# Kernel tuning notes

Measured on AMD Instinct MI355X. Metric: run time of the kernel, lower is better.

The kernel has to match this reference:

```python
import jax, jax.numpy as jnp
import numpy as np

CONF_THRES = 0.1
IOU_THRES = 0.6
MAX_DET = 300
MAX_WH = 4096.0  # class offset for non-agnostic NMS
NEG_SLOPE = 0.01  # nn.LeakyReLU default


def xywh2xyxy(p):
    xy, wh = p[..., :2], p[..., 2:4]
    return jnp.concatenate([xy - wh / 2, xy + wh / 2], axis=-1)


def pairwise_iou(a, b):
    area_a = (a[:, 2] - a[:, 0]) * (a[:, 3] - a[:, 1])
    area_b = (b[:, 2] - b[:, 0]) * (b[:, 3] - b[:, 1])
    lt = jnp.maximum(a[:, None, :2], b[None, :, :2])
    rb = jnp.minimum(a[:, None, 2:], b[None, :, 2:])
    wh = jnp.clip(rb - lt, 0.0)
    inter = wh[..., 0] * wh[..., 1]
    return inter / (area_a[:, None] + area_b[None, :] - inter + 1e-7)


def nms_single(pred):  # pred: [N, 5+nc]
    boxes = xywh2xyxy(pred[:, :4])
    scores = pred[:, 5:] * pred[:, 4:5]  # obj * cls
    conf = jnp.max(scores, axis=1)
    cls = jnp.argmax(scores, axis=1)
    conf = jnp.where(conf > CONF_THRES, conf, 0.0)
    topv, topi = jax.lax.top_k(conf, MAX_DET)
    b = boxes[topi]                      # [K,4]
    c = cls[topi]
    valid = topv > CONF_THRES
    bo = b + (c.astype(b.dtype) * MAX_WH)[:, None]  # class-offset boxes
    iou = pairwise_iou(bo, bo)           # [K,K]
    idx = jnp.arange(MAX_DET)
    def body(i, keep):
        sup = keep[i] & (iou[i] > IOU_THRES) & (idx > i)
        return keep & ~sup
    keep = jax.lax.fori_loop(0, MAX_DET, body, valid)
    return b, keep


def bilinear_sample(feat, y, x):  # feat [C,H,W], y/x [K,P] -> [C,K,P]
    C, H, W = feat.shape
    y = jnp.clip(y, 0.0, H - 1.0)
    x = jnp.clip(x, 0.0, W - 1.0)
    y0 = jnp.floor(y).astype(jnp.int32)
    x0 = jnp.floor(x).astype(jnp.int32)
    y1 = jnp.minimum(y0 + 1, H - 1)
    x1 = jnp.minimum(x0 + 1, W - 1)
    ly = y - y0
    lx = x - x0
    return (feat[:, y0, x0] * ((1 - ly) * (1 - lx))
            + feat[:, y0, x1] * ((1 - ly) * lx)
            + feat[:, y1, x0] * (ly * (1 - lx))
            + feat[:, y1, x1] * (ly * lx))


def roi_align_1x1(feat, boxes, scale):  # feat [C,H,W], boxes [K,4] xyxy (input-px)
    b = boxes * scale
    w = jnp.maximum(b[:, 2] - b[:, 0], 1.0)
    h = jnp.maximum(b[:, 3] - b[:, 1], 1.0)
    off = jnp.array([0.5, 1.5], dtype=boxes.dtype)
    xs = b[:, 0:1] + off[None, :] * (w[:, None] / 2.0)  # [K,2]
    ys = b[:, 1:2] + off[None, :] * (h[:, None] / 2.0)
    yy = ys[:, jnp.array([0, 0, 1, 1])]  # [K,4] 2x2 grid
    xx = xs[:, jnp.array([0, 1, 0, 1])]
    v = bilinear_sample(feat, yy, xx)    # [C,K,4]
    return jnp.mean(v, axis=2).T         # [K,C]


def rescale_boxes(bbox, hw, hw0):  # scale_coords + normalize by orig shape
    gain = jnp.minimum(hw[0] / hw0[0], hw[1] / hw0[1])
    pad_x = (hw[1] - hw0[1] * gain) / 2.0
    pad_y = (hw[0] - hw0[0] * gain) / 2.0
    x1 = jnp.clip((bbox[:, 0] - pad_x) / gain, 0.0, hw0[1])
    y1 = jnp.clip((bbox[:, 1] - pad_y) / gain, 0.0, hw0[0])
    x2 = jnp.clip((bbox[:, 2] - pad_x) / gain, 0.0, hw0[1])
    y2 = jnp.clip((bbox[:, 3] - pad_y) / gain, 0.0, hw0[0])
    # divide by shapes[i][0] indexed [w,h,w,h]
    return jnp.stack([x1 / hw0[1], y1 / hw0[0], x2 / hw0[1], y2 / hw0[0]], axis=1)


def setup_inputs() -> dict:
    key = jax.random.key(0)
    ks = jax.random.split(key, 10)
    B, N, NC = 8, 25500, 80
    xy = jax.random.uniform(ks[0], (B, N, 2), minval=0.0, maxval=640.0)
    wh = jax.random.uniform(ks[1], (B, N, 2), minval=8.0, maxval=160.0)
    obj = jax.random.uniform(ks[2], (B, N, 1))
    cls = jax.random.uniform(ks[3], (B, N, NC))
    preds = jnp.concatenate([xy, wh, obj, cls], axis=-1)
    feat1 = jax.random.normal(ks[4], (B, 128, 80, 80), dtype=jnp.float32)
    feat2 = jax.random.normal(ks[5], (B, 256, 40, 40), dtype=jnp.float32)
    feat3 = jax.random.normal(ks[6], (B, 512, 20, 20), dtype=jnp.float32)
    feat4 = jax.random.normal(ks[7], (B, 1024, 10, 10), dtype=jnp.float32)
    orig_hw = jnp.tile(jnp.array([[720.0, 1280.0]], dtype=jnp.float32), (B, 1))
    W1 = jax.random.normal(ks[8], (1920, 256), dtype=jnp.float32) * 0.02
    b1 = jnp.zeros((256,), dtype=jnp.float32)
    W2 = jax.random.normal(ks[9], (256, 256), dtype=jnp.float32) * 0.02
    b2 = jnp.zeros((256,), dtype=jnp.float32)
    return {"preds": preds, "feat1": feat1, "feat2": feat2, "feat3": feat3,
            "feat4": feat4, "orig_hw": orig_hw, "W1": W1, "b1": b1,
            "W2": W2, "b2": b2}


def reference(preds, feat1, feat2, feat3, feat4, orig_hw, W1, b1, W2, b2):
    preds = jax.lax.stop_gradient(preds)  # out.detach() in the original
    hw = jnp.array(feat1.shape[-2:], dtype=preds.dtype) * 8.0  # network input h,w
    boxes, keep = jax.vmap(nms_single)(preds)  # [B,K,4], [B,K]
    f1 = jax.vmap(lambda f, b: roi_align_1x1(f, b, 1.0 / 8))(feat1, boxes)
    f2 = jax.vmap(lambda f, b: roi_align_1x1(f, b, 1.0 / 16))(feat2, boxes)
    f3 = jax.vmap(lambda f, b: roi_align_1x1(f, b, 1.0 / 32))(feat3, boxes)
    f4 = jax.vmap(lambda f, b: roi_align_1x1(f, b, 1.0 / 64))(feat4, boxes)
    f = jnp.concatenate([f1, f2, f3, f4], axis=-1)  # [B,K,1920]
    h = jax.nn.leaky_relu(f @ W1 + b1, NEG_SLOPE)
    h = jax.nn.leaky_relu(h @ W2 + b2, NEG_SLOPE)   # [B,K,256]
    bb = jax.vmap(lambda b, s: rescale_boxes(b, hw, s))(boxes, orig_hw)
    out = jnp.concatenate([bb, h], axis=-1)  # [B,K,260]
    return out * keep[..., None].astype(out.dtype)
```

## Files before the change

### kernel.cpp

```cpp
#include <hip/hip_runtime.h>
#include <hip/hip_bf16.h>
#include <cstdint>
#include <cstddef>

#define NBATCH 8
#define NANCH 25500
#define MAXDET 300
#define NBINS 2048
#define CAP 2048

typedef __bf16 bf16x8 __attribute__((ext_vector_type(8)));
typedef float floatx4 __attribute__((ext_vector_type(4)));
typedef unsigned long long ull;

__device__ __forceinline__ int conf_bin(float v) {
  unsigned bits = __float_as_uint(v);
  int bin = (int)((bits - 0x3D800000u) >> 14);
  return bin > (NBINS - 1) ? (NBINS - 1) : bin;
}

#define CONF_TILE 64
__global__ __launch_bounds__(256) void conf_kernel(const float* __restrict__ preds,
                                                   float* __restrict__ conf,
                                                   int* __restrict__ cls, int total) {
  __shared__ float s[CONF_TILE * 85];
  int base = blockIdx.x * CONF_TILE;
  int nA = total - base; if (nA > CONF_TILE) nA = CONF_TILE;
  int n4 = (nA * 85) >> 2;
  const float4* g4 = (const float4*)(preds + (size_t)base * 85);
  float4* s4 = (float4*)s;
  for (int i = threadIdx.x; i < n4; i += 256) s4[i] = g4[i];
  __syncthreads();
  int lane16 = threadIdx.x & 15;
  int sub = threadIdx.x >> 4;
  #pragma unroll
  for (int r = 0; r < 4; ++r) {
    int a = r * 16 + sub;
    if (a < nA) {
      const float* row = s + a * 85;
      float obj = row[4];
      float best = -1.0f; int bc = 0;
      #pragma unroll
      for (int j = 0; j < 5; ++j) {
        int c = lane16 * 5 + j;
        float v = row[5 + c] * obj;
        if (v > best) { best = v; bc = c; }
      }
      #pragma unroll
      for (int m = 1; m < 16; m <<= 1) {
        float ov = __shfl_xor(best, m, 64);
        int   oc = __shfl_xor(bc,   m, 64);
        if (ov > best || (ov == best && oc < bc)) { best = ov; bc = oc; }
      }
      if (lane16 == 0) {
        int idx = base + a;
        conf[idx] = (best > 0.1f) ? best : 0.0f;
        cls[idx] = bc;
      }
    }
  }
}

struct TransArgs {
  const float* src[6];
  __hip_bfloat16* dst[6];
  int C[6], HW[6], tx[6], tpb[6], start[6];
};

__global__ __launch_bounds__(1024) void mid_kernel(TransArgs a,
                                                   const float* __restrict__ conf,
                                                   const float* __restrict__ preds,
                                                   const int* __restrict__ clsg,
                                                   float* __restrict__ cand_v, int* __restrict__ cand_i,
                                                   float* __restrict__ boxesWs, int* __restrict__ keepWs,
                                                   const float* __restrict__ orig_hw,
                                                   float* __restrict__ out,
                                                   int n_trans_tiles) {
  #pragma clang fp contract(off)
  __shared__ __align__(16) char smem[69632];
  int bid = blockIdx.x;
  int t = threadIdx.y * 32 + threadIdx.x;

  if (bid >= 8) {
    int wv = t >> 6, l = t & 63;
    int wid = (bid - 8) * 16 + wv;
    int wtot = ((int)gridDim.x - 8) * 16;
    float* tile = (float*)(smem + wv * 4352);
    for (int gt = wid; gt < n_trans_tiles; gt += wtot) {
      int s = 0;
      #pragma unroll
      for (int i = 1; i < 6; ++i) if (gt >= a.start[i]) s = i;
      int local = gt - a.start[s];
      int C = a.C[s], HW = a.HW[s], tx0 = a.tx[s], tpb = a.tpb[s];
      int bb = local / tpb;
      int rem = local - bb * tpb;
      int p0 = (rem % tx0) * 32;
      int c0 = (rem / tx0) * 32;
      const float* inb = a.src[s] + (size_t)bb * C * HW;
      __hip_bfloat16* outb = a.dst[s] + (size_t)bb * C * HW;
      if (p0 + 32 <= HW) {
        #pragma unroll
        for (int k = 0; k < 4; ++k) {
          int cr = k * 8 + (l >> 3);
          int pr = (l & 7) * 4;
          float4 v = *(const float4*)(inb + (size_t)(c0 + cr) * HW + p0 + pr);
          float* d = tile + cr * 33 + pr;
          d[0] = v.x; d[1] = v.y; d[2] = v.z; d[3] = v.w;
        }
        asm volatile("s_waitcnt lgkmcnt(0)" ::: "memory");
        __builtin_amdgcn_sched_barrier(0);
        #pragma unroll
        for (int k = 0; k < 16; ++k) {
          int pr = k * 2 + (l >> 5);
          int cr = l & 31;
          outb[(size_t)(p0 + pr) * C + c0 + cr] = __float2bfloat16(tile[cr * 33 + pr]);
        }
      } else {
        int nvp = HW - p0;
        #pragma unroll
        for (int k = 0; k < 4; ++k) {
          int cr = k * 8 + (l >> 3);
          int pr = (l & 7) * 4;
          const float* src = inb + (size_t)(c0 + cr) * HW + p0;
          float* d = tile + cr * 33 + pr;
          #pragma unroll
          for (int j = 0; j < 4; ++j) d[j] = (pr + j < nvp) ? src[pr + j] : 0.0f;
        }
        asm volatile("s_waitcnt lgkmcnt(0)" ::: "memory");
        __builtin_amdgcn_sched_barrier(0);
        #pragma unroll
        for (int k = 0; k < 16; ++k) {
          int pr = k * 2 + (l >> 5);
          int cr = l & 31;
          if (pr < nvp) outb[(size_t)(p0 + pr) * C + c0 + cr] = __float2bfloat16(tile[cr * 33 + pr]);
        }
      }
    }
    return;
  }

  int b = bid;
  int*    s_h  = (int*)smem;
  int*    s_ctr= (int*)(smem + 8192);
  ull   (*mask)[5] = (ull(*)[5])smem;
  float*  lv_s = (float*)(smem + 16384);
  int*    li_s = (int*)(smem + 24576);
  float4* bo4  = (float4*)(smem + 32768);
  float (*bxx)[4] = (float(*)[4])(smem + 37568);
  ull* keepw = (ull*)(smem + 42368);
  ull* nzrow = (ull*)(smem + 42408);
  int* shv   = (int*)(smem + 42448);

  s_h[t] = 0; s_h[t + 1024] = 0;
  if (t < 300) {
    bo4[t] = make_float4(0.0f, 0.0f, 0.0f, 0.0f);
    bxx[t][0] = 0.0f; bxx[t][1] = 0.0f; bxx[t][2] = 0.0f; bxx[t][3] = 0.0f;
  }
  if (t < 5) nzrow[t] = 0ULL;
  if (t == 1) { shv[0] = NBINS; shv[2] = 0; }
  __syncthreads();

  {
    const float4* cf4 = (const float4*)(conf + (size_t)b * NANCH);
    const int N4 = NANCH >> 2;
    for (int i = t; i < N4; i += 1024) {
      float4 v = cf4[i];
      if (v.x > 0.1f) atomicAdd(&s_h[conf_bin(v.x)], 1);
      if (v.y > 0.1f) atomicAdd(&s_h[conf_bin(v.y)], 1);
      if (v.z > 0.1f) atomicAdd(&s_h[conf_bin(v.z)], 1);
      if (v.w > 0.1f) atomicAdd(&s_h[conf_bin(v.w)], 1);
    }
  }
  __syncthreads();

  int r[8], suf[8], rs[8];
  int w = t >> 6, lane = t & 63;
  if (t < 256) {
    #pragma unroll
    for (int k = 0; k < 8; ++k)
      r[k] = s_h[(w * 8 + k) * 64 + lane];
    int bsum = 0;
    #pragma unroll
    for (int k = 0; k < 8; ++k) {
      int s = r[k];
      #pragma unroll
      for (int d = 1; d < 64; d <<= 1) {
        int o = __shfl_down(s, d, 64);
        if (lane + d < 64) s += o;
      }
      suf[k] = s - r[k];
      rs[k] = __shfl(s, 0, 64);
      bsum += rs[k];
    }
    if (lane == 0) shv[4 + w] = bsum;
  }
  __syncthreads();
  if (t < 256) {
    int p1 = shv[5], p2 = shv[6], p3 = shv[7];
    int total = shv[4] + p1 + p2 + p3;
    int target = total < 300 ? total : 300;
    int RS = (w == 0) ? (p1 + p2 + p3) : (w == 1) ? (p2 + p3) : (w == 2) ? p3 : 0;
    int run = RS;
    #pragma unroll
    for (int k = 7; k >= 0; --k) {
      int Sx = run + suf[k] + r[k];
      int Sx1 = Sx - r[k];
      int bin = (w * 8 + k) * 64 + lane;
      s_h[bin] = Sx;
      s_ctr[bin] = Sx1;
      if (total > 0 && Sx >= target && Sx1 < target) { shv[0] = bin; shv[2] = Sx; }
      run += rs[k];
    }
    if (t == 0) shv[1] = total;
  }
  __syncthreads();
  int T = shv[0];
  int total = shv[1];
  int Kslots = shv[2];
  int nvalid = total < 300 ? total : 300;

  if (t >= nvalid && t < 300) {
    size_t bi = ((size_t)(b * 300 + t)) * 4;
    boxesWs[bi + 0] = 0.0f; boxesWs[bi + 1] = 0.0f;
    boxesWs[bi + 2] = 0.0f; boxesWs[bi + 3] = 0.0f;
  }
  if (t < 5) {
    int n = nvalid - t * 64;
    keepw[t] = (n <= 0) ? 0ULL : (n >= 64 ? ~0ULL : ((1ULL << n) - 1ULL));
  }

  {
    const float4* cf4 = (const float4*)(conf + (size_t)b * NANCH);
    const int N4 = NANCH >> 2;
    float* cv = cand_v + (size_t)b * NANCH;
    int*   ci = cand_i + (size_t)b * NANCH;
    if (total > 0) {
      for (int i4 = t; i4 < N4; i4 += 1024) {
        float4 v4 = cf4[i4];
        int i0 = i4 * 4;
        float vv[4] = {v4.x, v4.y, v4.z, v4.w};
        #pragma unroll
        for (int q = 0; q < 4; ++q) {
          float v = vv[q];
          if (v > 0.1f) {
            int bin = conf_bin(v);
            if (bin >= T) {
              int slot = atomicAdd(&s_ctr[bin], 1);
              if (slot < CAP) { lv_s[slot] = v; li_s[slot] = i0 + q; }
              else            { cv[slot] = v;   ci[slot] = i0 + q;   }
            }
          }
        }
      }
    }
  }
  __syncthreads();

  {
    const float* cv = cand_v + (size_t)b * NANCH;
    const int*   ci = cand_i + (size_t)b * NANCH;
    for (int sIdx = t; sIdx < Kslots; sIdx += 1024) {
      float v; int id;
      if (sIdx < CAP) { v = lv_s[sIdx]; id = li_s[sIdx]; }
      else            { v = cv[sIdx];   id = ci[sIdx];   }
      int bin = conf_bin(v);
      int lo = (bin + 1 < NBINS) ? s_h[bin + 1] : 0;
      int hi = s_h[bin];
      int rank = lo;
      for (int j = lo; j < hi; ++j) {
        float vj; int ij;
        if (j < CAP) { vj = lv_s[j]; ij = li_s[j]; }
        else         { vj = cv[j];   ij = ci[j];   }
        rank += (int)((vj > v) | ((vj == v) & (ij < id)));
      }
      if (rank < 300) {
        const float* p = preds + ((size_t)b * NANCH + id) * 85;
        float cx = p[0], cy = p[1], wq = p[2], hq = p[3];
        float hw2 = wq * 0.5f, hh2 = hq * 0.5f;
        float x1 = cx - hw2, y1 = cy - hh2, x2 = cx + hw2, y2 = cy + hh2;
        bxx[rank][0] = x1; bxx[rank][1] = y1; bxx[rank][2] = x2; bxx[rank][3] = y2;
        size_t bi = ((size_t)(b * 300 + rank)) * 4;
        boxesWs[bi + 0] = x1; boxesWs[bi + 1] = y1;
        boxesWs[bi + 2] = x2; boxesWs[bi + 3] = y2;
        int c = clsg[(size_t)b * NANCH + id];
        float off = (float)c * 4096.0f;
        float4 ob; ob.x = x1 + off; ob.y = y1 + off; ob.z = x2 + off; ob.w = y2 + off;
        bo4[rank] = ob;
      }
    }
  }
  __syncthreads();

  {
    int wv2 = t >> 6, ln = t & 63;
    if (wv2 < 10) {
      int w2 = wv2 >> 1, half = wv2 & 1;
      int j = w2 * 64 + ln;
      int jc = j < 300 ? j : 0;
      float4 jb = bo4[jc];
      float ja = (jb.z - jb.x) * (jb.w - jb.y);
      bool jv = j < 300;
      int iend = w2 * 64 + 64; if (iend > 300) iend = 300;
      int i0 = half * 150, i1 = i0 + 150; if (i1 > iend) i1 = iend;
      #pragma unroll 4
      for (int i = i0; i < i1; ++i) {
        float4 ib = bo4[i];
        float ai = (ib.z - ib.x) * (ib.w - ib.y);
        float ltx = fmaxf(ib.x, jb.x);
        float lty = fmaxf(ib.y, jb.y);
        float rbx = fminf(ib.z, jb.z);
        float rby = fminf(ib.w, jb.w);
        float wx = fmaxf(rbx - ltx, 0.0f);
        float wy = fmaxf(rby - lty, 0.0f);
        float inter = wx * wy;
        float iou = inter / (ai + ja - inter + 1e-7f);
        ull bal = __ballot(jv && (j > i) && (iou > 0.6f));
        if (ln == 0) {
          mask[i][w2] = bal;
          if (bal) atomicOr(&nzrow[i >> 6], 1ULL << (i & 63));
        }
      }
    }
  }
  __syncthreads();
  if (t == 0) {
    ull kw[5], nz[5];
    #pragma unroll
    for (int w2 = 0; w2 < 5; ++w2) { kw[w2] = keepw[w2]; nz[w2] = nzrow[w2]; }
    #pragma unroll
    for (int w2 = 0; w2 < 5; ++w2) {
      ull p = kw[w2] & nz[w2];
      while (p) {
        int l2 = __builtin_ctzll(p);
        p &= p - 1;
        int i = w2 * 64 + l2;
        for (int w3 = w2; w3 < 5; ++w3) {
          ull m = mask[i][w3];
          kw[w3] &= ~m;
          if (w3 == w2) p &= ~m;
        }
      }
    }
    #pragma unroll
    for (int w2 = 0; w2 < 5; ++w2) keepw[w2] = kw[w2];
  }
  __syncthreads();
  if (t < 300) {
    int kp = (int)((keepw[t >> 6] >> (t & 63)) & 1ULL);
    keepWs[b * 300 + t] = kp;
    float oh = orig_hw[b * 2 + 0], ow = orig_hw[b * 2 + 1];
    float gain = fminf(640.0f / oh, 640.0f / ow);
    float padx = (640.0f - ow * gain) * 0.5f;
    float pady = (640.0f - oh * gain) * 0.5f;
    float x1 = fminf(fmaxf((bxx[t][0] - padx) / gain, 0.0f), ow) / ow;
    float y1 = fminf(fmaxf((bxx[t][1] - pady) / gain, 0.0f), oh) / oh;
    float x2 = fminf(fmaxf((bxx[t][2] - padx) / gain, 0.0f), ow) / ow;
    float y2 = fminf(fmaxf((bxx[t][3] - pady) / gain, 0.0f), oh) / oh;
    size_t o = ((size_t)(b * 300 + t)) * 260;
    out[o + 0] = kp ? x1 : 0.0f;
    out[o + 1] = kp ? y1 : 0.0f;
    out[o + 2] = kp ? x2 : 0.0f;
    out[o + 3] = kp ? y2 : 0.0f;
  }
}

__global__ __launch_bounds__(256) void roi_kernel(const float* __restrict__ boxes,
                                                  const __hip_bfloat16* __restrict__ fT1, const __hip_bfloat16* __restrict__ fT2,
                                                  const __hip_bfloat16* __restrict__ fT3, const __hip_bfloat16* __restrict__ fT4,
                                                  __hip_bfloat16* __restrict__ f) {
  int b = blockIdx.x & 7;
  int r = blockIdx.x >> 3;
  __shared__ int t_off[4][16];
  __shared__ float t_w[4][16];
  int t = threadIdx.x;
  const int Hs[4] = {80, 40, 20, 10};
  const int Cs[4] = {128, 256, 512, 1024};
  const float ss[4] = {0.125f, 0.0625f, 0.03125f, 0.015625f};
  size_t bbase = ((size_t)(b * 300 + r)) * 4;
  float bx0 = boxes[bbase + 0];
  float by0 = boxes[bbase + 1];
  float bx1 = boxes[bbase + 2];
  float by1 = boxes[bbase + 3];
  if (t < 64) {
    int lv = t >> 4, k = t & 15, pp = k >> 2, nb = k & 3;
    float s = ss[lv];
    int H = Hs[lv], W = Hs[lv], C = Cs[lv];
    float b0 = bx0 * s, b1 = by0 * s, b2 = bx1 * s, b3 = by1 * s;
    float w = fmaxf(b2 - b0, 1.0f), h = fmaxf(b3 - b1, 1.0f);
    const float offv[2] = {0.5f, 1.5f};
    float px = b0 + offv[pp & 1] * (w * 0.5f);
    float py = b1 + offv[pp >> 1] * (h * 0.5f);
    float y = fminf(fmaxf(py, 0.0f), (float)(H - 1));
    float x = fminf(fmaxf(px, 0.0f), (float)(W - 1));
    int y0 = (int)floorf(y), x0 = (int)floorf(x);
    int y1 = min(y0 + 1, H - 1), x1 = min(x0 + 1, W - 1);
    float ly = y - (float)y0, lx = x - (float)x0;
    int yy = (nb & 2) ? y1 : y0;
    int xx = (nb & 1) ? x1 : x0;
    float wy = (nb & 2) ? ly : (1.0f - ly);
    float wx = (nb & 1) ? lx : (1.0f - lx);
    t_off[lv][k] = (yy * W + xx) * C;
    t_w[lv][k] = wy * wx;
  }
  __syncthreads();
  const __hip_bfloat16* bases[4] = {
    fT1 + (size_t)b * 6400 * 128,
    fT2 + (size_t)b * 1600 * 256,
    fT3 + (size_t)b * 400 * 512,
    fT4 + (size_t)b * 100 * 1024
  };
  __hip_bfloat16* frow = f + (size_t)(b * 300 + r) * 1920;
  int cbase = 0;
  #pragma unroll
  for (int lv = 0; lv < 4; ++lv) {
    int C = Cs[lv];
    const __hip_bfloat16* base = bases[lv];
    for (int c = t; c < C; c += 256) {
      float acc = 0.0f;
      #pragma unroll
      for (int k = 0; k < 16; ++k)
        acc += t_w[lv][k] * __bfloat162float(base[t_off[lv][k] + c]);
      frow[cbase + c] = __float2bfloat16(acc * 0.25f);
    }
    cbase += C;
  }
}

#define GLDS16(gp, lp) __builtin_amdgcn_global_load_lds( \
    (const __attribute__((address_space(1))) unsigned int*)(gp), \
    (__attribute__((address_space(3))) unsigned int*)(lp), 16, 0, 0)

__global__ __launch_bounds__(256) void gemm_tile_kernel(const __hip_bfloat16* __restrict__ A,
                                                        const __hip_bfloat16* __restrict__ BT,
                                                        const float* __restrict__ bias,
                                                        __hip_bfloat16* __restrict__ Cb,
                                                        float* __restrict__ Cf,
                                                        const int* __restrict__ keep,
                                                        int M, int N, int K, int ldc, int coff) {
  __shared__ __hip_bfloat16 sA[2][64 * 64];
  __shared__ __hip_bfloat16 sB[2][64 * 64];
  int tid = threadIdx.x;
  int bm = blockIdx.x * 64, bn = blockIdx.y * 64;
  int wave = tid >> 6, lane = tid & 63;
  int wr = wave >> 1, wc = wave & 1;
  int idx16 = lane & 15, kb = lane >> 4;
  floatx4 acc[2][2] = {};
  int nt = K >> 6;

  auto stage = [&](int buf, int t) {
    int k0 = t << 6;
    #pragma unroll
    for (int i = 0; i < 2; ++i) {
      int c = tid + i * 256;
      int row = c >> 3, cc = c & 7;
      int scc = cc ^ (row & 7);
      GLDS16(A + (size_t)(bm + row) * K + k0 + scc * 8,
             (char*)&sA[buf][0] + c * 16);
    }
    #pragma unroll
    for (int i = 0; i < 2; ++i) {
      int c = tid + i * 256;
      int row = c >> 3, cc = c & 7;
      int scc = cc ^ (row & 7);
      GLDS16(BT + (size_t)(bn + row) * K + k0 + scc * 8,
             (char*)&sB[buf][0] + c * 16);
    }
  };

  stage(0, 0);
  asm volatile("s_waitcnt vmcnt(0)" ::: "memory");
  __syncthreads();
  int cur = 0;
  for (int t = 0; t < nt; ++t) {
    if (t + 1 < nt) stage(cur ^ 1, t + 1);
    const char* Ab = (const char*)&sA[cur][0];
    const char* Bb = (const char*)&sB[cur][0];
    #pragma unroll
    for (int s = 0; s < 2; ++s) {
      bf16x8 af[2], bg[2];
      #pragma unroll
      for (int m = 0; m < 2; ++m) {
        int row = wr * 32 + m * 16 + idx16;
        int chunk = s * 4 + kb;
        af[m] = *(const bf16x8*)(Ab + row * 128 + ((chunk ^ (row & 7)) * 16));
      }
      #pragma unroll
      for (int n = 0; n < 2; ++n) {
        int row = wc * 32 + n * 16 + idx16;
        int chunk = s * 4 + kb;
        bg[n] = *(const bf16x8*)(Bb + row * 128 + ((chunk ^ (row & 7)) * 16));
      }
      #pragma unroll
      for (int m = 0; m < 2; ++m)
        #pragma unroll
        for (int n = 0; n < 2; ++n)
          acc[m][n] = __builtin_amdgcn_mfma_f32_16x16x32_bf16(af[m], bg[n], acc[m][n], 0, 0, 0);
    }
    asm volatile("s_waitcnt vmcnt(0)" ::: "memory");
    __syncthreads();
    cur ^= 1;
  }
  int col = lane & 15, rb4 = (lane >> 4) * 4;
  #pragma unroll
  for (int m = 0; m < 2; ++m) {
    #pragma unroll
    for (int n = 0; n < 2; ++n) {
      #pragma unroll
      for (int r = 0; r < 4; ++r) {
        int orow = bm + wr * 32 + m * 16 + rb4 + r;
        int ocol = bn + wc * 32 + n * 16 + col;
        if (orow >= M) continue;
        float v = acc[m][n][r] + bias[ocol];
        v = (v >= 0.0f) ? v : 0.01f * v;
        if (Cb) Cb[(size_t)orow * N + ocol] = __float2bfloat16(v);
        if (Cf) {
          float km = keep ? (keep[orow] ? 1.0f : 0.0f) : 1.0f;
          Cf[(size_t)orow * ldc + coff + ocol] = v * km;
        }
      }
    }
  }
}

extern "C" void kernel_launch(void* const* d_in, const int* in_sizes, int n_in,
                              void* d_out, int out_size, void* d_ws, size_t ws_size,
                              hipStream_t stream) {
  (void)in_sizes; (void)n_in; (void)out_size; (void)ws_size;
  const float* preds  = (const float*)d_in[0];
  const float* feat1  = (const float*)d_in[1];
  const float* feat2  = (const float*)d_in[2];
  const float* feat3  = (const float*)d_in[3];
  const float* feat4  = (const float*)d_in[4];
  const float* orighw = (const float*)d_in[5];
  const float* W1     = (const float*)d_in[6];
  const float* b1     = (const float*)d_in[7];
  const float* W2     = (const float*)d_in[8];
  const float* b2     = (const float*)d_in[9];
  float* out = (float*)d_out;

  char* ws = (char*)d_ws;
  size_t off = 0;
  auto alloc = [&](size_t bytes) -> void* {
    void* p = ws + off;
    off = (off + bytes + 255) & ~(size_t)255;
    return p;
  };
  const int BN = NBATCH * NANCH;
  float*  conf   = (float*)alloc((size_t)BN * 4);
  int*    cls    = (int*)  alloc((size_t)BN * 4);
  float*  cand_v = (float*)alloc((size_t)BN * 4);
  int*    cand_i = (int*)  alloc((size_t)BN * 4);
  float*  boxes  = (float*)alloc((size_t)NBATCH * 300 * 4 * 4);
  int*    keep   = (int*)  alloc((size_t)NBATCH * 300 * 4);
  __hip_bfloat16* fT1  = (__hip_bfloat16*)alloc((size_t)NBATCH * 6400 * 128 * 2);
  __hip_bfloat16* fT2  = (__hip_bfloat16*)alloc((size_t)NBATCH * 1600 * 256 * 2);
  __hip_bfloat16* fT3  = (__hip_bfloat16*)alloc((size_t)NBATCH * 400 * 512 * 2);
  __hip_bfloat16* fT4  = (__hip_bfloat16*)alloc((size_t)NBATCH * 100 * 1024 * 2);
  __hip_bfloat16* fmat = (__hip_bfloat16*)alloc((size_t)2400 * 1920 * 2);
  __hip_bfloat16* h1b  = (__hip_bfloat16*)alloc((size_t)2400 * 256 * 2);
  __hip_bfloat16* W1T  = (__hip_bfloat16*)alloc((size_t)256 * 1920 * 2);
  __hip_bfloat16* W2T  = (__hip_bfloat16*)alloc((size_t)256 * 256 * 2);

  conf_kernel<<<(BN + CONF_TILE - 1) / CONF_TILE, 256, 0, stream>>>(preds, conf, cls, BN);

  TransArgs ta;
  ta.src[0] = feat1; ta.dst[0] = fT1; ta.C[0] = 128;  ta.HW[0] = 6400; ta.tx[0] = 200;
  ta.src[1] = feat2; ta.dst[1] = fT2; ta.C[1] = 256;  ta.HW[1] = 1600; ta.tx[1] = 50;
  ta.src[2] = feat3; ta.dst[2] = fT3; ta.C[2] = 512;  ta.HW[2] = 400;  ta.tx[2] = 13;
  ta.src[3] = feat4; ta.dst[3] = fT4; ta.C[3] = 1024; ta.HW[3] = 100;  ta.tx[3] = 4;
  ta.src[4] = W1;    ta.dst[4] = W1T; ta.C[4] = 1920; ta.HW[4] = 256;  ta.tx[4] = 8;
  ta.src[5] = W2;    ta.dst[5] = W2T; ta.C[5] = 256;  ta.HW[5] = 256;  ta.tx[5] = 8;
  int n_tiles = 0;
  for (int s = 0; s < 6; ++s) {
    int ty = (ta.C[s] + 31) / 32;
    int nbatch = (s < 4) ? NBATCH : 1;
    ta.tpb[s] = ta.tx[s] * ty;
    ta.start[s] = n_tiles;
    n_tiles += ta.tpb[s] * nbatch;
  }
  mid_kernel<<<8 + 432, dim3(32, 32), 0, stream>>>(ta, conf, preds, cls,
                                                   cand_v, cand_i, boxes, keep, orighw, out,
                                                   n_tiles);

  roi_kernel<<<2400, 256, 0, stream>>>(boxes, fT1, fT2, fT3, fT4, fmat);
  gemm_tile_kernel<<<dim3(38, 4), 256, 0, stream>>>(fmat, W1T, b1, h1b, nullptr, nullptr,
                                                    2400, 256, 1920, 0, 0);
  gemm_tile_kernel<<<dim3(38, 4), 256, 0, stream>>>(h1b, W2T, b2, nullptr, out, keep,
                                                    2400, 256, 256, 260, 4);
}
```

Before: 121.0 us.

## Move histogram into conf kernel and parallelize candidate scatter across helper blocks

The per-batch confidence histogram is now built with global atomics inside the conf kernel instead of by one block per batch in the mid kernel. 64 new helper blocks (8 per batch) each compute the threshold bin and scatter the candidates from one segment into bin-sorted global slots, packing score, index, class and box into 64-bit words. The NMS blocks spin on a per-batch counter until the helpers finish, then rank the candidates from global memory. This removes the serial 25.5k-element scan done by a single block per batch. In exchange it adds a memset, global atomics, an inter-block spin-wait that assumes the helper blocks are co-resident, and atomic reads of global memory during ranking.

```diff
diff --git a/kernel.cpp b/kernel.cpp
--- a/kernel.cpp
+++ b/kernel.cpp
@@ -7,7 +7,10 @@
 #define NANCH 25500
 #define MAXDET 300
 #define NBINS 2048
-#define CAP 2048
+#define NMS_BLKS 8
+#define SCAT_BLKS 64
+#define TRANS_BASE (NMS_BLKS + SCAT_BLKS)
+#define TRANS_BLKS 376
 
 typedef __bf16 bf16x8 __attribute__((ext_vector_type(8)));
 typedef float floatx4 __attribute__((ext_vector_type(4)));
@@ -22,7 +25,8 @@
 #define CONF_TILE 64
 __global__ __launch_bounds__(256) void conf_kernel(const float* __restrict__ preds,
                                                    float* __restrict__ conf,
-                                                   int* __restrict__ cls, int total) {
+                                                   int* __restrict__ cls,
+                                                   int* __restrict__ ghist, int total) {
   __shared__ float s[CONF_TILE * 85];
   int base = blockIdx.x * CONF_TILE;
   int nA = total - base; if (nA > CONF_TILE) nA = CONF_TILE;
@@ -54,8 +58,13 @@
       }
       if (lane16 == 0) {
         int idx = base + a;
-        conf[idx] = (best > 0.1f) ? best : 0.0f;
+        bool pass = best > 0.1f;
+        conf[idx] = pass ? best : 0.0f;
         cls[idx] = bc;
+        if (pass) {
+          int b = idx / NANCH;
+          atomicAdd(&ghist[b * NBINS + conf_bin(best)], 1);
+        }
       }
     }
   }
@@ -71,7 +80,12 @@
                                                    const float* __restrict__ conf,
                                                    const float* __restrict__ preds,
                                                    const int* __restrict__ clsg,
-                                                   float* __restrict__ cand_v, int* __restrict__ cand_i,
+                                                   const int* __restrict__ ghist,
+                                                   int* __restrict__ gcnt,
+                                                   int* __restrict__ ctr2,
+                                                   ull* __restrict__ gA,
+                                                   ull* __restrict__ gB,
+                                                   ull* __restrict__ gC,
                                                    float* __restrict__ boxesWs, int* __restrict__ keepWs,
                                                    const float* __restrict__ orig_hw,
                                                    float* __restrict__ out,
@@ -81,10 +95,10 @@
   int bid = blockIdx.x;
   int t = threadIdx.y * 32 + threadIdx.x;
 
-  if (bid >= 8) {
+  if (bid >= TRANS_BASE) {
     int wv = t >> 6, l = t & 63;
-    int wid = (bid - 8) * 16 + wv;
-    int wtot = ((int)gridDim.x - 8) * 16;
+    int wid = (bid - TRANS_BASE) * 16 + wv;
+    int wtot = ((int)gridDim.x - TRANS_BASE) * 16;
     float* tile = (float*)(smem + wv * 4352);
     for (int gt = wid; gt < n_trans_tiles; gt += wtot) {
       int s = 0;
@@ -139,82 +153,142 @@
     return;
   }
 
+  if (bid >= NMS_BLKS) {
+    int hb = bid - NMS_BLKS;
+    int b = hb >> 3, seg = hb & 7;
+    int* s_suf = (int*)smem;
+    int* shv   = (int*)(smem + 8192);
+    int r[8], suf[8], rs[8];
+    int w = t >> 6, lane = t & 63;
+    if (t == 0) shv[0] = NBINS;
+    if (t < 256) {
+      #pragma unroll
+      for (int k = 0; k < 8; ++k)
+        r[k] = ghist[b * NBINS + (w * 8 + k) * 64 + lane];
+      int bsum = 0;
+      #pragma unroll
+      for (int k = 0; k < 8; ++k) {
+        int s = r[k];
+        #pragma unroll
+        for (int d = 1; d < 64; d <<= 1) {
+          int o = __shfl_down(s, d, 64);
+          if (lane + d < 64) s += o;
+        }
+        suf[k] = s - r[k];
+        rs[k] = __shfl(s, 0, 64);
+        bsum += rs[k];
+      }
+      if (lane == 0) shv[4 + w] = bsum;
+    }
+    __syncthreads();
+    if (t < 256) {
+      int p1 = shv[5], p2 = shv[6], p3 = shv[7];
+      int total = shv[4] + p1 + p2 + p3;
+      int target = total < 300 ? total : 300;
+      int RS = (w == 0) ? (p1 + p2 + p3) : (w == 1) ? (p2 + p3) : (w == 2) ? p3 : 0;
+      int run = RS;
+      #pragma unroll
+      for (int k = 7; k >= 0; --k) {
+        int Sx = run + suf[k] + r[k];
+        int Sx1 = Sx - r[k];
+        int bin = (w * 8 + k) * 64 + lane;
+        s_suf[bin] = Sx1;
+        if (total > 0 && Sx >= target && Sx1 < target) shv[0] = bin;
+        run += rs[k];
+      }
+    }
+    __syncthreads();
+    int T = shv[0];
+    const int N4 = NANCH >> 2;
+    int i0 = (N4 * seg) >> 3, i1 = (N4 * (seg + 1)) >> 3;
+    const float4* cf4 = (const float4*)(conf + (size_t)b * NANCH);
+    for (int i = i0 + t; i < i1; i += 1024) {
+      float4 v4 = cf4[i];
+      int ib = i * 4;
+      float vv[4] = {v4.x, v4.y, v4.z, v4.w};
+      #pragma unroll
+      for (int q = 0; q < 4; ++q) {
+        float v = vv[q];
+        if (v > 0.1f) {
+          int bin = conf_bin(v);
+          if (bin >= T) {
+            int slot = s_suf[bin] + atomicAdd(&gcnt[b * NBINS + bin], 1);
+            int idx = ib + q;
+            const float* p = preds + ((size_t)b * NANCH + idx) * 85;
+            float cx = p[0], cy = p[1], wq = p[2], hq = p[3];
+            float hw2 = wq * 0.5f, hh2 = hq * 0.5f;
+            float x1 = cx - hw2, y1 = cy - hh2, x2 = cx + hw2, y2 = cy + hh2;
+            int c = clsg[(size_t)b * NANCH + idx];
+            size_t g = (size_t)b * NANCH + slot;
+            atomicExch(&gA[g], ((ull)__float_as_uint(v) << 32) | (unsigned)(idx | (c << 20)));
+            atomicExch(&gB[g], ((ull)__float_as_uint(x1) << 32) | __float_as_uint(y1));
+            atomicExch(&gC[g], ((ull)__float_as_uint(x2) << 32) | __float_as_uint(y2));
+          }
+        }
+      }
+    }
+    __syncthreads();
+    if (t == 0) { __threadfence(); atomicAdd(&ctr2[b], 1); }
+    return;
+  }
+
   int b = bid;
   int*    s_h  = (int*)smem;
-  int*    s_ctr= (int*)(smem + 8192);
-  ull   (*mask)[5] = (ull(*)[5])smem;
-  float*  lv_s = (float*)(smem + 16384);
-  int*    li_s = (int*)(smem + 24576);
-  float4* bo4  = (float4*)(smem + 32768);
-  float (*bxx)[4] = (float(*)[4])(smem + 37568);
-  ull* keepw = (ull*)(smem + 42368);
-  ull* nzrow = (ull*)(smem + 42408);
-  int* shv   = (int*)(smem + 42448);
-
-  s_h[t] = 0; s_h[t + 1024] = 0;
+  float4* bo4  = (float4*)(smem + 8192);
+  float (*bxx)[4] = (float(*)[4])(smem + 12992);
+  ull   (*mask)[5] = (ull(*)[5])(smem + 17792);
+  ull* keepw = (ull*)(smem + 29792);
+  ull* nzrow = (ull*)(smem + 29832);
+  int* shv   = (int*)(smem + 29872);
+
   if (t < 300) {
     bo4[t] = make_float4(0.0f, 0.0f, 0.0f, 0.0f);
     bxx[t][0] = 0.0f; bxx[t][1] = 0.0f; bxx[t][2] = 0.0f; bxx[t][3] = 0.0f;
   }
   if (t < 5) nzrow[t] = 0ULL;
-  if (t == 1) { shv[0] = NBINS; shv[2] = 0; }
-  __syncthreads();
-
+  if (t == 0) { shv[0] = NBINS; shv[2] = 0; }
   {
-    const float4* cf4 = (const float4*)(conf + (size_t)b * NANCH);
-    const int N4 = NANCH >> 2;
-    for (int i = t; i < N4; i += 1024) {
-      float4 v = cf4[i];
-      if (v.x > 0.1f) atomicAdd(&s_h[conf_bin(v.x)], 1);
-      if (v.y > 0.1f) atomicAdd(&s_h[conf_bin(v.y)], 1);
-      if (v.z > 0.1f) atomicAdd(&s_h[conf_bin(v.z)], 1);
-      if (v.w > 0.1f) atomicAdd(&s_h[conf_bin(v.w)], 1);
-    }
-  }
-  __syncthreads();
-
-  int r[8], suf[8], rs[8];
-  int w = t >> 6, lane = t & 63;
-  if (t < 256) {
-    #pragma unroll
-    for (int k = 0; k < 8; ++k)
-      r[k] = s_h[(w * 8 + k) * 64 + lane];
-    int bsum = 0;
-    #pragma unroll
-    for (int k = 0; k < 8; ++k) {
-      int s = r[k];
-      #pragma unroll
-      for (int d = 1; d < 64; d <<= 1) {
-        int o = __shfl_down(s, d, 64);
-        if (lane + d < 64) s += o;
-      }
-      suf[k] = s - r[k];
-      rs[k] = __shfl(s, 0, 64);
-      bsum += rs[k];
-    }
-    if (lane == 0) shv[4 + w] = bsum;
-  }
-  __syncthreads();
-  if (t < 256) {
-    int p1 = shv[5], p2 = shv[6], p3 = shv[7];
-    int total = shv[4] + p1 + p2 + p3;
-    int target = total < 300 ? total : 300;
-    int RS = (w == 0) ? (p1 + p2 + p3) : (w == 1) ? (p2 + p3) : (w == 2) ? p3 : 0;
-    int run = RS;
-    #pragma unroll
-    for (int k = 7; k >= 0; --k) {
-      int Sx = run + suf[k] + r[k];
-      int Sx1 = Sx - r[k];
-      int bin = (w * 8 + k) * 64 + lane;
-      s_h[bin] = Sx;
-      s_ctr[bin] = Sx1;
-      if (total > 0 && Sx >= target && Sx1 < target) { shv[0] = bin; shv[2] = Sx; }
-      run += rs[k];
-    }
-    if (t == 0) shv[1] = total;
-  }
-  __syncthreads();
-  int T = shv[0];
+    int r[8], suf[8], rs[8];
+    int w = t >> 6, lane = t & 63;
+    if (t < 256) {
+      #pragma unroll
+      for (int k = 0; k < 8; ++k)
+        r[k] = ghist[b * NBINS + (w * 8 + k) * 64 + lane];
+      int bsum = 0;
+      #pragma unroll
+      for (int k = 0; k < 8; ++k) {
+        int s = r[k];
+        #pragma unroll
+        for (int d = 1; d < 64; d <<= 1) {
+          int o = __shfl_down(s, d, 64);
+          if (lane + d < 64) s += o;
+        }
+        suf[k] = s - r[k];
+        rs[k] = __shfl(s, 0, 64);
+        bsum += rs[k];
+      }
+      if (lane == 0) shv[4 + w] = bsum;
+    }
+    __syncthreads();
+    if (t < 256) {
+      int p1 = shv[5], p2 = shv[6], p3 = shv[7];
+      int total = shv[4] + p1 + p2 + p3;
+      int target = total < 300 ? total : 300;
+      int RS = (w == 0) ? (p1 + p2 + p3) : (w == 1) ? (p2 + p3) : (w == 2) ? p3 : 0;
+      int run = RS;
+      #pragma unroll
+      for (int k = 7; k >= 0; --k) {
+        int Sx = run + suf[k] + r[k];
+        int Sx1 = Sx - r[k];
+        int bin = (w * 8 + k) * 64 + lane;
+        s_h[bin] = Sx;
+        if (total > 0 && Sx >= target && Sx1 < target) { shv[0] = bin; shv[2] = Sx; }
+        run += rs[k];
+      }
+      if (t == 0) shv[1] = total;
+    }
+  }
+  __syncthreads();
   int total = shv[1];
   int Kslots = shv[2];
   int nvalid = total < 300 ? total : 300;
@@ -228,65 +302,45 @@
     int n = nvalid - t * 64;
     keepw[t] = (n <= 0) ? 0ULL : (n >= 64 ? ~0ULL : ((1ULL << n) - 1ULL));
   }
-
-  {
-    const float4* cf4 = (const float4*)(conf + (size_t)b * NANCH);
-    const int N4 = NANCH >> 2;
-    float* cv = cand_v + (size_t)b * NANCH;
-    int*   ci = cand_i + (size_t)b * NANCH;
-    if (total > 0) {
-      for (int i4 = t; i4 < N4; i4 += 1024) {
-        float4 v4 = cf4[i4];
-        int i0 = i4 * 4;
-        float vv[4] = {v4.x, v4.y, v4.z, v4.w};
-        #pragma unroll
-        for (int q = 0; q < 4; ++q) {
-          float v = vv[q];
-          if (v > 0.1f) {
-            int bin = conf_bin(v);
-            if (bin >= T) {
-              int slot = atomicAdd(&s_ctr[bin], 1);
-              if (slot < CAP) { lv_s[slot] = v; li_s[slot] = i0 + q; }
-              else            { cv[slot] = v;   ci[slot] = i0 + q;   }
-            }
-          }
-        }
-      }
-    }
-  }
-  __syncthreads();
-
-  {
-    const float* cv = cand_v + (size_t)b * NANCH;
-    const int*   ci = cand_i + (size_t)b * NANCH;
-    for (int sIdx = t; sIdx < Kslots; sIdx += 1024) {
-      float v; int id;
-      if (sIdx < CAP) { v = lv_s[sIdx]; id = li_s[sIdx]; }
-      else            { v = cv[sIdx];   id = ci[sIdx];   }
-      int bin = conf_bin(v);
-      int lo = (bin + 1 < NBINS) ? s_h[bin + 1] : 0;
-      int hi = s_h[bin];
-      int rank = lo;
-      for (int j = lo; j < hi; ++j) {
-        float vj; int ij;
-        if (j < CAP) { vj = lv_s[j]; ij = li_s[j]; }
-        else         { vj = cv[j];   ij = ci[j];   }
-        rank += (int)((vj > v) | ((vj == v) & (ij < id)));
-      }
-      if (rank < 300) {
-        const float* p = preds + ((size_t)b * NANCH + id) * 85;
-        float cx = p[0], cy = p[1], wq = p[2], hq = p[3];
-        float hw2 = wq * 0.5f, hh2 = hq * 0.5f;
-        float x1 = cx - hw2, y1 = cy - hh2, x2 = cx + hw2, y2 = cy + hh2;
-        bxx[rank][0] = x1; bxx[rank][1] = y1; bxx[rank][2] = x2; bxx[rank][3] = y2;
-        size_t bi = ((size_t)(b * 300 + rank)) * 4;
-        boxesWs[bi + 0] = x1; boxesWs[bi + 1] = y1;
-        boxesWs[bi + 2] = x2; boxesWs[bi + 3] = y2;
-        int c = clsg[(size_t)b * NANCH + id];
-        float off = (float)c * 4096.0f;
-        float4 ob; ob.x = x1 + off; ob.y = y1 + off; ob.z = x2 + off; ob.w = y2 + off;
-        bo4[rank] = ob;
-      }
+  if (t == 0) {
+    while (atomicAdd(&ctr2[b], 0) < 8) __builtin_amdgcn_s_sleep(8);
+    __threadfence();
+  }
+  __syncthreads();
+
+  for (int sIdx = t; sIdx < Kslots; sIdx += 1024) {
+    ull aA = atomicAdd(&gA[(size_t)b * NANCH + sIdx], 0ULL);
+    float v = __uint_as_float((unsigned)(aA >> 32));
+    unsigned code = (unsigned)aA;
+    int id = (int)(code & 0xFFFFFu);
+    int bin = conf_bin(v);
+    int lo = (bin + 1 < NBINS) ? s_h[bin + 1] : 0;
+    int hi = s_h[bin];
+    int rank = lo;
+    #pragma unroll 4
+    for (int j = lo; j < hi; ++j) {
+      ull aj = atomicAdd(&gA[(size_t)b * NANCH + j], 0ULL);
+      float vj = __uint_as_float((unsigned)(aj >> 32));
+      int ij = (int)((unsigned)aj & 0xFFFFFu);
+      int gt = vj > v;
+      int eq = (vj == v) & (ij < id);
+      rank += gt | eq;
+    }
+    if (rank < 300) {
+      ull pb = atomicAdd(&gB[(size_t)b * NANCH + sIdx], 0ULL);
+      ull pc = atomicAdd(&gC[(size_t)b * NANCH + sIdx], 0ULL);
+      float x1 = __uint_as_float((unsigned)(pb >> 32));
+      float y1 = __uint_as_float((unsigned)pb);
+      float x2 = __uint_as_float((unsigned)(pc >> 32));
+      float y2 = __uint_as_float((unsigned)pc);
+      bxx[rank][0] = x1; bxx[rank][1] = y1; bxx[rank][2] = x2; bxx[rank][3] = y2;
+      size_t bi = ((size_t)(b * 300 + rank)) * 4;
+      boxesWs[bi + 0] = x1; boxesWs[bi + 1] = y1;
+      boxesWs[bi + 2] = x2; boxesWs[bi + 3] = y2;
+      int c = (int)((code >> 20) & 0x7Fu);
+      float off = (float)c * 4096.0f;
+      float4 ob; ob.x = x1 + off; ob.y = y1 + off; ob.z = x2 + off; ob.w = y2 + off;
+      bo4[rank] = ob;
     }
   }
   __syncthreads();
@@ -548,8 +602,12 @@
   const int BN = NBATCH * NANCH;
   float*  conf   = (float*)alloc((size_t)BN * 4);
   int*    cls    = (int*)  alloc((size_t)BN * 4);
-  float*  cand_v = (float*)alloc((size_t)BN * 4);
-  int*    cand_i = (int*)  alloc((size_t)BN * 4);
+  ull*    gA     = (ull*)  alloc((size_t)BN * 8);
+  ull*    gB     = (ull*)  alloc((size_t)BN * 8);
+  ull*    gC     = (ull*)  alloc((size_t)BN * 8);
+  int*    ghist  = (int*)  alloc((size_t)NBATCH * NBINS * 4);
+  int*    gcnt   = (int*)  alloc((size_t)NBATCH * NBINS * 4);
+  int*    ctr2   = (int*)  alloc(256);
   float*  boxes  = (float*)alloc((size_t)NBATCH * 300 * 4 * 4);
   int*    keep   = (int*)  alloc((size_t)NBATCH * 300 * 4);
   __hip_bfloat16* fT1  = (__hip_bfloat16*)alloc((size_t)NBATCH * 6400 * 128 * 2);
@@ -561,7 +619,9 @@
   __hip_bfloat16* W1T  = (__hip_bfloat16*)alloc((size_t)256 * 1920 * 2);
   __hip_bfloat16* W2T  = (__hip_bfloat16*)alloc((size_t)256 * 256 * 2);
 
-  conf_kernel<<<(BN + CONF_TILE - 1) / CONF_TILE, 256, 0, stream>>>(preds, conf, cls, BN);
+  hipMemsetAsync(ghist, 0, (size_t)NBATCH * NBINS * 4 * 2 + 256, stream);
+
+  conf_kernel<<<(BN + CONF_TILE - 1) / CONF_TILE, 256, 0, stream>>>(preds, conf, cls, ghist, BN);
 
   TransArgs ta;
   ta.src[0] = feat1; ta.dst[0] = fT1; ta.C[0] = 128;  ta.HW[0] = 6400; ta.tx[0] = 200;
@@ -578,9 +638,11 @@
     ta.start[s] = n_tiles;
     n_tiles += ta.tpb[s] * nbatch;
   }
-  mid_kernel<<<8 + 432, dim3(32, 32), 0, stream>>>(ta, conf, preds, cls,
-                                                   cand_v, cand_i, boxes, keep, orighw, out,
-                                                   n_tiles);
+  mid_kernel<<<TRANS_BASE + TRANS_BLKS, dim3(32, 32), 0, stream>>>(ta, conf, preds, cls,
+                                                                   ghist, gcnt, ctr2,
+                                                                   gA, gB, gC,
+                                                                   boxes, keep, orighw, out,
+                                                                   n_tiles);
 
   roi_kernel<<<2400, 256, 0, stream>>>(boxes, fT1, fT2, fT3, fT4, fmat);
   gemm_tile_kernel<<<dim3(38, 4), 256, 0, stream>>>(fmat, W1T, b1, h1b, nullptr, nullptr,
```

Result: slower. 135.6 us (+12.1%).
